# Performance work log

Hardware: AMD Instinct MI355X
Metric: run time of the kernel (lower is better)

## Reference

```python
import jax, jax.numpy as jnp
import numpy as np
from functools import partial

ALPHA = 0.99   # EMA smoothing factor of unbiasedExponentialSmoother
EPS = 1e-5

def setup_inputs() -> dict:
    key = jax.random.key(0)
    B, C, T = 8, 256, 16384
    x = jax.random.normal(key, (B, C, T), dtype=jnp.float32)
    return {"x": x}

def _causal_unbiased_ema_norm(x, alpha, eps):
    # x: [B, C, T]. Causal instance norm: per (b, c) lane, running unbiased
    # EMA estimates of mean and second moment over time, then normalize.
    B, C, T = x.shape
    xt = jnp.transpose(x, (2, 0, 1))  # [T, B, C] time-major for scan

    def step(carry, xi):
        s1, s2, w = carry
        s1 = alpha * s1 + (1.0 - alpha) * xi          # EMA of x
        s2 = alpha * s2 + (1.0 - alpha) * xi * xi     # EMA of x^2
        w = alpha * w + (1.0 - alpha)                 # bias correction 1-alpha^t
        mean = s1 / w
        var = s2 / w - mean * mean
        out = (xi - mean) * jax.lax.rsqrt(var + eps)
        return (s1, s2, w), out

    z = jnp.zeros((B, C), dtype=x.dtype)
    w0 = jnp.zeros((), dtype=x.dtype)
    _, yt = jax.lax.scan(step, (z, z, w0), xt)
    return jnp.transpose(yt, (1, 2, 0))  # back to [B, C, T]

def reference(x):
    # MyInstanceNorm1d(causal=True, use_unbiasEMA=True, affine=False):
    # permute/unsqueeze wrapper around the causal unbiased-EMA smoother.
    return _causal_unbiased_ema_norm(x, ALPHA, EPS)
```

## Files before the change

kernel.cpp:

```cpp
#include <hip/hip_runtime.h>

#define T_LEN  16384
#define NTHR   384
#define NWAVE  6
#define SEGS   4
#define TOT4   1536
#define PAD4(i) ((i) + ((i) >> 4))


__device__ __forceinline__ void process16(const float4* __restrict__ xv,
                                          float4* __restrict__ yv,
                                          float s1, float s2, float w) {
    const float A    = 0.99f;
    const float OMA  = (float)(1.0 - 0.99);
    const float EPSF = 1e-5f;
#pragma unroll
    for (int i = 0; i < 4; ++i) {
        float4 xq = xv[i];
        float4 oq;
#pragma unroll
        for (int e = 0; e < 4; ++e) {
            float xi = (e == 0) ? xq.x : (e == 1) ? xq.y : (e == 2) ? xq.z : xq.w;
            float t = OMA * xi;
            s1 = fmaf(A, s1, t);
            s2 = fmaf(A, s2, t * xi);
            w  = fmaf(A, w, OMA);
            float numer = fmaf(xi, w, -s1);
            float arg   = fmaf(s2, w, fmaf(-s1, s1, EPSF * (w * w)));
            float rs    = __builtin_amdgcn_rsqf(arg);
            float o     = numer * rs;
            if (e == 0) oq.x = o; else if (e == 1) oq.y = o; else if (e == 2) oq.z = o; else oq.w = o;
        }
        yv[i] = oq;
    }
}

__global__ __launch_bounds__(NTHR, 8)
void ema_norm_kernel(const float* __restrict__ x, float* __restrict__ y) {
    const float A   = 0.99f;
    const float OMA = (float)(1.0 - 0.99);
    const float Kf  = (float)((double)((float)(1.0 - 0.99)) / (1.0 - (double)0.99f));

    const int o   = (blockIdx.x & 7) * 1024 + (blockIdx.x >> 3);
    const int row = o >> 2;
    const int seg = o & 3;

    const int tid  = threadIdx.x;
    const int lane = tid & 63;
    const int wid  = tid >> 6;

    const float4* __restrict__ xr4 = reinterpret_cast<const float4*>(x + (size_t)row * T_LEN);
    float4*       __restrict__ yr4 = reinterpret_cast<float4*>(y + (size_t)row * T_LEN);

    __shared__ float4 buf[TOT4 + TOT4 / 16];
    __shared__ float  tW1[NWAVE], tW2[NWAVE];

    const int base4 = seg * 1024 - 512;

#pragma unroll
    for (int k = 0; k < 4; ++k) {
        int i = tid + NTHR * k;
        int g = base4 + i;
        float4 v = make_float4(0.f, 0.f, 0.f, 0.f);
        if (g >= 0) v = xr4[g];
        buf[PAD4(i)] = v;
    }
    __syncthreads();

    float4 xv[4];
#pragma unroll
    for (int c = 0; c < 4; ++c) { int i = 4 * tid + c; xv[c] = buf[PAD4(i)]; }

    float s1 = 0.f, s2 = 0.f;
#pragma unroll
    for (int i = 0; i < 4; ++i) {
        float t;
        t = OMA * xv[i].x; s1 = fmaf(A, s1, t); s2 = fmaf(A, s2, t * xv[i].x);
        t = OMA * xv[i].y; s1 = fmaf(A, s1, t); s2 = fmaf(A, s2, t * xv[i].y);
        t = OMA * xv[i].z; s1 = fmaf(A, s1, t); s2 = fmaf(A, s2, t * xv[i].z);
        t = OMA * xv[i].w; s1 = fmaf(A, s1, t); s2 = fmaf(A, s2, t * xv[i].w);
    }

    float a16 = A;
#pragma unroll
    for (int i = 0; i < 4; ++i) a16 *= a16;
    float d[10];
    d[0] = a16;
#pragma unroll
    for (int k = 1; k < 10; ++k) d[k] = d[k - 1] * d[k - 1];

    float v1 = s1, v2 = s2;
#pragma unroll
    for (int k = 0; k < 6; ++k) {
        const int off = 1 << k;
        float o1 = __shfl_up(v1, off, 64);
        float o2 = __shfl_up(v2, off, 64);
        if (lane >= off) { v1 = fmaf(d[k], o1, v1); v2 = fmaf(d[k], o2, v2); }
    }
    float c1 = __shfl_up(v1, 1, 64);
    float c2 = __shfl_up(v2, 1, 64);
    if (lane == 0) { c1 = 0.f; c2 = 0.f; }

    if (lane == 63) { tW1[wid] = v1; tW2[wid] = v2; }
    __syncthreads();
    float W1 = 0.f, W2 = 0.f;
    const float Dw = d[6];
    for (int v = 0; v < wid; ++v) {
        W1 = fmaf(W1, Dw, tW1[v]);
        W2 = fmaf(W2, Dw, tW2[v]);
    }
    float fdec = 1.f;
#pragma unroll
    for (int k = 0; k < 6; ++k) if (lane & (1 << k)) fdec *= d[k];
    c1 = fmaf(W1, fdec, c1);
    c2 = fmaf(W2, fdec, c2);

    const int m = 256 * seg - 128 + tid;
    float w0 = 0.f;
    if (m > 0) {
        float pw = 1.f;
#pragma unroll
        for (int k = 0; k < 10; ++k) if (m & (1 << k)) pw *= d[k];
        w0 = Kf * (1.f - pw);
    }

    float4 ov[4];
    process16(xv, ov, c1, c2, w0);
#pragma unroll
    for (int c = 0; c < 4; ++c) { int i = 4 * tid + c; buf[PAD4(i)] = ov[c]; }
    __syncthreads();

#pragma unroll
    for (int k = 0; k < 3; ++k) {
        int i = tid + NTHR * k;
        if (i < 1024) {
            int s = 512 + i;
            yr4[seg * 1024 + i] = buf[PAD4(s)];
        }
    }
}

extern "C" void kernel_launch(void* const* d_in, const int* in_sizes, int n_in,
                              void* d_out, int out_size, void* d_ws, size_t ws_size,
                              hipStream_t stream) {
    const float* x = (const float*)d_in[0];
    float* y = (float*)d_out;
    const int rows = in_sizes[0] / T_LEN;
    ema_norm_kernel<<<rows * SEGS, NTHR, 0, stream>>>(x, y);
}
```

Before: 233.4 us.

## Process whole row per block with carried scan state and register prefetch

The kernel no longer splits each row into four overlapping segments, each of which recomputed a 512-float4 warm-up halo. Each block now walks one full row in four sequential 1024-float4 chunks, carrying the EMA state across chunks and prefetching the next chunk into registers while the current one is processed. This removes the redundant halo loads and compute (about 1.5x the reads before), but it cuts the grid from 8192 blocks to 2048 and serialises chunks within a block, adding barriers and reducing parallelism.

```diff
diff --git a/kernel.cpp b/kernel.cpp
--- a/kernel.cpp
+++ b/kernel.cpp
@@ -1,16 +1,14 @@
 #include <hip/hip_runtime.h>
 
 #define T_LEN  16384
-#define NTHR   384
-#define NWAVE  6
-#define SEGS   4
-#define TOT4   1536
+#define NTHR   256
+#define NWAVE  4
+#define CH4    1024
+#define ROW4   4096
 #define PAD4(i) ((i) + ((i) >> 4))
 
 
-__device__ __forceinline__ void process16(const float4* __restrict__ xv,
-                                          float4* __restrict__ yv,
-                                          float s1, float s2, float w) {
+__device__ __forceinline__ void process16(float4 (&xv)[4], float s1, float s2, float w) {
     const float A    = 0.99f;
     const float OMA  = (float)(1.0 - 0.99);
     const float EPSF = 1e-5f;
@@ -31,55 +29,25 @@
             float o     = numer * rs;
             if (e == 0) oq.x = o; else if (e == 1) oq.y = o; else if (e == 2) oq.z = o; else oq.w = o;
         }
-        yv[i] = oq;
+        xv[i] = oq;
     }
 }
 
 __global__ __launch_bounds__(NTHR, 8)
 void ema_norm_kernel(const float* __restrict__ x, float* __restrict__ y) {
     const float A   = 0.99f;
-    const float OMA = (float)(1.0 - 0.99);
     const float Kf  = (float)((double)((float)(1.0 - 0.99)) / (1.0 - (double)0.99f));
 
-    const int o   = (blockIdx.x & 7) * 1024 + (blockIdx.x >> 3);
-    const int row = o >> 2;
-    const int seg = o & 3;
-
+    const int row  = blockIdx.x;
     const int tid  = threadIdx.x;
     const int lane = tid & 63;
     const int wid  = tid >> 6;
 
-    const float4* __restrict__ xr4 = reinterpret_cast<const float4*>(x + (size_t)row * T_LEN);
-    float4*       __restrict__ yr4 = reinterpret_cast<float4*>(y + (size_t)row * T_LEN);
+    const float4* __restrict__ xr4 = reinterpret_cast<const float4*>(x) + (size_t)row * ROW4;
+    float4*       __restrict__ yr4 = reinterpret_cast<float4*>(y) + (size_t)row * ROW4;
 
-    __shared__ float4 buf[TOT4 + TOT4 / 16];
+    __shared__ float4 buf[CH4 + CH4 / 16];
     __shared__ float  tW1[NWAVE], tW2[NWAVE];
-
-    const int base4 = seg * 1024 - 512;
-
-#pragma unroll
-    for (int k = 0; k < 4; ++k) {
-        int i = tid + NTHR * k;
-        int g = base4 + i;
-        float4 v = make_float4(0.f, 0.f, 0.f, 0.f);
-        if (g >= 0) v = xr4[g];
-        buf[PAD4(i)] = v;
-    }
-    __syncthreads();
-
-    float4 xv[4];
-#pragma unroll
-    for (int c = 0; c < 4; ++c) { int i = 4 * tid + c; xv[c] = buf[PAD4(i)]; }
-
-    float s1 = 0.f, s2 = 0.f;
-#pragma unroll
-    for (int i = 0; i < 4; ++i) {
-        float t;
-        t = OMA * xv[i].x; s1 = fmaf(A, s1, t); s2 = fmaf(A, s2, t * xv[i].x);
-        t = OMA * xv[i].y; s1 = fmaf(A, s1, t); s2 = fmaf(A, s2, t * xv[i].y);
-        t = OMA * xv[i].z; s1 = fmaf(A, s1, t); s2 = fmaf(A, s2, t * xv[i].z);
-        t = OMA * xv[i].w; s1 = fmaf(A, s1, t); s2 = fmaf(A, s2, t * xv[i].w);
-    }
 
     float a16 = A;
 #pragma unroll
@@ -88,56 +56,88 @@
     d[0] = a16;
 #pragma unroll
     for (int k = 1; k < 10; ++k) d[k] = d[k - 1] * d[k - 1];
+    const float Dw = d[6];
 
-    float v1 = s1, v2 = s2;
-#pragma unroll
-    for (int k = 0; k < 6; ++k) {
-        const int off = 1 << k;
-        float o1 = __shfl_up(v1, off, 64);
-        float o2 = __shfl_up(v2, off, 64);
-        if (lane >= off) { v1 = fmaf(d[k], o1, v1); v2 = fmaf(d[k], o2, v2); }
-    }
-    float c1 = __shfl_up(v1, 1, 64);
-    float c2 = __shfl_up(v2, 1, 64);
-    if (lane == 0) { c1 = 0.f; c2 = 0.f; }
-
-    if (lane == 63) { tW1[wid] = v1; tW2[wid] = v2; }
-    __syncthreads();
-    float W1 = 0.f, W2 = 0.f;
-    const float Dw = d[6];
-    for (int v = 0; v < wid; ++v) {
-        W1 = fmaf(W1, Dw, tW1[v]);
-        W2 = fmaf(W2, Dw, tW2[v]);
-    }
     float fdec = 1.f;
 #pragma unroll
     for (int k = 0; k < 6; ++k) if (lane & (1 << k)) fdec *= d[k];
-    c1 = fmaf(W1, fdec, c1);
-    c2 = fmaf(W2, fdec, c2);
+    float pwtid = 1.f;
+#pragma unroll
+    for (int k = 0; k < 8; ++k) if (tid & (1 << k)) pwtid *= d[k];
 
-    const int m = 256 * seg - 128 + tid;
-    float w0 = 0.f;
-    if (m > 0) {
-        float pw = 1.f;
+    float C1 = 0.f, C2 = 0.f;
+
+    float4 rA[4], rB[4];
 #pragma unroll
-        for (int k = 0; k < 10; ++k) if (m & (1 << k)) pw *= d[k];
-        w0 = Kf * (1.f - pw);
-    }
+    for (int k = 0; k < 4; ++k) rA[k] = xr4[tid + NTHR * k];
 
-    float4 ov[4];
-    process16(xv, ov, c1, c2, w0);
+    auto do_iter = [&](float4 (&rc)[4], float4 (&rn)[4], int it, float pwit, bool prefetch) {
+        if (prefetch) {
 #pragma unroll
-    for (int c = 0; c < 4; ++c) { int i = 4 * tid + c; buf[PAD4(i)] = ov[c]; }
-    __syncthreads();
+            for (int k = 0; k < 4; ++k) rn[k] = xr4[(it + 1) * CH4 + tid + NTHR * k];
+        }
+#pragma unroll
+        for (int k = 0; k < 4; ++k) buf[PAD4(tid + NTHR * k)] = rc[k];
+        __syncthreads();
 
+        float4 xv[4];
 #pragma unroll
-    for (int k = 0; k < 3; ++k) {
-        int i = tid + NTHR * k;
-        if (i < 1024) {
-            int s = 512 + i;
-            yr4[seg * 1024 + i] = buf[PAD4(s)];
+        for (int c = 0; c < 4; ++c) xv[c] = buf[PAD4(4 * tid + c)];
+        const float OMA = (float)(1.0 - 0.99);
+        float s1 = 0.f, s2 = 0.f;
+#pragma unroll
+        for (int i = 0; i < 4; ++i) {
+            float t;
+            t = OMA * xv[i].x; s1 = fmaf(A, s1, t); s2 = fmaf(A, s2, t * xv[i].x);
+            t = OMA * xv[i].y; s1 = fmaf(A, s1, t); s2 = fmaf(A, s2, t * xv[i].y);
+            t = OMA * xv[i].z; s1 = fmaf(A, s1, t); s2 = fmaf(A, s2, t * xv[i].z);
+            t = OMA * xv[i].w; s1 = fmaf(A, s1, t); s2 = fmaf(A, s2, t * xv[i].w);
         }
-    }
+
+        float v1 = s1, v2 = s2;
+#pragma unroll
+        for (int k = 0; k < 6; ++k) {
+            const int off = 1 << k;
+            float o1 = __shfl_up(v1, off, 64);
+            float o2 = __shfl_up(v2, off, 64);
+            if (lane >= off) { v1 = fmaf(d[k], o1, v1); v2 = fmaf(d[k], o2, v2); }
+        }
+        float c1 = __shfl_up(v1, 1, 64);
+        float c2 = __shfl_up(v2, 1, 64);
+        if (lane == 0) { c1 = 0.f; c2 = 0.f; }
+
+        if (lane == 63) { tW1[wid] = v1; tW2[wid] = v2; }
+        __syncthreads();
+        float W1 = C1, W2 = C2;
+        float myW1 = C1, myW2 = C2;
+#pragma unroll
+        for (int v = 0; v < NWAVE; ++v) {
+            if (v == wid) { myW1 = W1; myW2 = W2; }
+            W1 = fmaf(Dw, W1, tW1[v]);
+            W2 = fmaf(Dw, W2, tW2[v]);
+        }
+        C1 = W1; C2 = W2;
+        c1 = fmaf(myW1, fdec, c1);
+        c2 = fmaf(myW2, fdec, c2);
+
+        float w0 = Kf * (1.f - pwtid * pwit);
+
+        process16(xv, c1, c2, w0);
+#pragma unroll
+        for (int c = 0; c < 4; ++c) buf[PAD4(4 * tid + c)] = xv[c];
+        __syncthreads();
+#pragma unroll
+        for (int k = 0; k < 4; ++k) yr4[it * CH4 + tid + NTHR * k] = buf[PAD4(tid + NTHR * k)];
+        __syncthreads();
+    };
+
+    const float p1 = d[8];
+    const float p2 = d[9];
+    const float p3 = d[8] * d[9];
+    do_iter(rA, rB, 0, 1.0f, true);
+    do_iter(rB, rA, 1, p1,   true);
+    do_iter(rA, rB, 2, p2,   true);
+    do_iter(rB, rA, 3, p3,   false);
 }
 
 extern "C" void kernel_launch(void* const* d_in, const int* in_sizes, int n_in,
@@ -146,5 +146,5 @@
     const float* x = (const float*)d_in[0];
     float* y = (float*)d_out;
     const int rows = in_sizes[0] / T_LEN;
-    ema_norm_kernel<<<rows * SEGS, NTHR, 0, stream>>>(x, y);
+    ema_norm_kernel<<<rows, NTHR, 0, stream>>>(x, y);
 }
```

Measured after the change: 296.2 us. 1.27x slower.
